# Kernel optimization log

Hardware: AMD Instinct MI355X
Metric: run time of the kernel (lower is better)

## Reference

```python
import jax, jax.numpy as jnp
import numpy as np


def setup_inputs() -> dict:
    key = jax.random.key(0)
    k1, k2 = jax.random.split(key)
    B, H, W = 16, 1024, 1024
    NB = 20
    preds = jax.random.randint(k1, (B, H, W), 0, NB, dtype=jnp.int32)
    targets = jax.random.randint(k2, (B, H, W), 0, NB, dtype=jnp.int32)
    return {"preds": preds, "targets": targets, "nb_class": NB, "smooth": 1}


def reference(preds, targets, nb_class, smooth):
    # Single-pass histogram formulation of the per-class IoU loop:
    #   intersection[c] = #{pred==c and target==c}
    #   union[c]        = #{pred==c} + #{target==c} - intersection[c]
    p = preds.reshape(-1)
    t = targets.reshape(-1)
    pred_count = jnp.bincount(p, length=nb_class).astype(jnp.float32)
    target_count = jnp.bincount(t, length=nb_class).astype(jnp.float32)
    # pixels where pred==target contribute to intersection of that class
    match = p == t
    intersection = jnp.bincount(jnp.where(match, p, nb_class), length=nb_class + 1)[:nb_class].astype(jnp.float32)
    union = pred_count + target_count - intersection
    s = jnp.float32(smooth)
    iou_per_class = (intersection + s) / (union + s)  # [nb_class]
    mIoU = iou_per_class.mean()
    return 1.0 - mIoU
```

## Files before the change

kernel.cpp:

```cpp
#include <hip/hip_runtime.h>
#include <hip/hip_bf16.h>


#define NB      20
#define BLK     256
#define GRID_H  1024
#define PSTRIDE 64

__device__ __forceinline__ void dma16(const void* g, void* l) {
    __builtin_amdgcn_global_load_lds(
        (const __attribute__((address_space(1))) unsigned*)g,
        (__attribute__((address_space(3))) unsigned*)l, 16, 0, 0);
}

__device__ __forceinline__ void process_pix(int p, int t, unsigned* s_col) {
    unsigned m = (unsigned)(p == t);
    atomicAdd(&s_col[p * BLK], 1u + (m << 20));
    atomicAdd(&s_col[t * BLK], 1u << 10);
}

__device__ __forceinline__ void process_vec(int4 pv, int4 tv, unsigned* s_col) {
    process_pix(pv.x, tv.x, s_col);
    process_pix(pv.y, tv.y, s_col);
    process_pix(pv.z, tv.z, s_col);
    process_pix(pv.w, tv.w, s_col);
}

__global__ __launch_bounds__(BLK) void miou_hist_kernel(
        const int4* __restrict__ preds, const int4* __restrict__ targs,
        unsigned* __restrict__ partials, int n4, int full_iters) {
    __shared__ unsigned s_hist[NB * BLK];
    __shared__ int4 s_p[2][BLK];
    __shared__ int4 s_t[2][BLK];
    const int tid  = threadIdx.x;
    const int wid  = tid >> 6;
    const int lane = tid & 63;

    #pragma unroll
    for (int c = 0; c < NB; ++c) s_hist[c * BLK + tid] = 0u;
    __syncthreads();

    unsigned* s_col = &s_hist[tid];
    const int CHUNK = gridDim.x * BLK;
    const int base  = blockIdx.x * BLK + tid;

    if (full_iters >= 2) {
        dma16(&preds[base],         &s_p[0][wid * 64]);
        dma16(&targs[base],         &s_t[0][wid * 64]);
        dma16(&preds[base + CHUNK], &s_p[1][wid * 64]);
        dma16(&targs[base + CHUNK], &s_t[1][wid * 64]);

        for (int j = 0; j < full_iters - 1; ++j) {
            const int slot = j & 1;
            asm volatile("s_waitcnt vmcnt(2)" ::: "memory");
            int4 pv = s_p[slot][wid * 64 + lane];
            int4 tv = s_t[slot][wid * 64 + lane];
            asm volatile("s_waitcnt lgkmcnt(0)" ::: "memory");
            if (j + 2 < full_iters) {
                dma16(&preds[base + (j + 2) * CHUNK], &s_p[slot][wid * 64]);
                dma16(&targs[base + (j + 2) * CHUNK], &s_t[slot][wid * 64]);
            }
            process_vec(pv, tv, s_col);
        }
        {
            const int slot = (full_iters - 1) & 1;
            asm volatile("s_waitcnt vmcnt(0)" ::: "memory");
            int4 pv = s_p[slot][wid * 64 + lane];
            int4 tv = s_t[slot][wid * 64 + lane];
            process_vec(pv, tv, s_col);
        }
    }
    for (int i = base + full_iters * CHUNK; i < n4; i += CHUNK) {
        int4 pv = preds[i];
        int4 tv = targs[i];
        process_vec(pv, tv, s_col);
    }
    __syncthreads();

    unsigned* dst = &partials[(size_t)blockIdx.x * PSTRIDE];
    for (int c = wid; c < NB; c += (BLK / 64)) {
        unsigned sp = 0, st = 0, si = 0;
        #pragma unroll
        for (int k = 0; k < BLK / 64; ++k) {
            unsigned v = s_hist[c * BLK + k * 64 + lane];
            sp += v & 1023u;
            st += (v >> 10) & 1023u;
            si += (v >> 20) & 1023u;
        }
        #pragma unroll
        for (int off = 32; off > 0; off >>= 1) {
            sp += __shfl_xor(sp, off);
            st += __shfl_xor(st, off);
            si += __shfl_xor(si, off);
        }
        if (lane == 0) {
            dst[c]          = sp;
            dst[NB + c]     = st;
            dst[2 * NB + c] = si;
        }
    }
}

__global__ __launch_bounds__(1024) void miou_reduce_kernel(
        const unsigned* __restrict__ partials, int nblocks,
        const int* __restrict__ nb_ptr, const int* __restrict__ smooth_ptr,
        float* __restrict__ out) {
    __shared__ unsigned s_tot[PSTRIDE];
    if (threadIdx.x < PSTRIDE) s_tot[threadIdx.x] = 0u;
    __syncthreads();

    const int col4 = threadIdx.x & 15;
    const int seg  = threadIdx.x >> 4;
    const int4* p4 = (const int4*)partials;

    unsigned ax = 0, ay = 0, az = 0, aw = 0;
    #pragma unroll 8
    for (int r = seg; r < nblocks; r += 64) {
        int4 v = p4[r * 16 + col4];
        ax += (unsigned)v.x; ay += (unsigned)v.y;
        az += (unsigned)v.z; aw += (unsigned)v.w;
    }
    atomicAdd(&s_tot[col4 * 4 + 0], ax);
    atomicAdd(&s_tot[col4 * 4 + 1], ay);
    atomicAdd(&s_tot[col4 * 4 + 2], az);
    atomicAdd(&s_tot[col4 * 4 + 3], aw);
    __syncthreads();

    if (threadIdx.x == 0) {
        const int   nb = *nb_ptr;
        const float s  = (float)(*smooth_ptr);
        float acc_iou = 0.0f;
        for (int c = 0; c < nb && c < NB; ++c) {
            float pc    = (float)s_tot[c];
            float tc    = (float)s_tot[NB + c];
            float inter = (float)s_tot[2 * NB + c];
            float uni   = pc + tc - inter;
            acc_iou += (inter + s) / (uni + s);
        }
        out[0] = 1.0f - acc_iou / (float)nb;
    }
}

extern "C" void kernel_launch(void* const* d_in, const int* in_sizes, int n_in,
                              void* d_out, int out_size, void* d_ws, size_t ws_size,
                              hipStream_t stream) {
    const int4* preds      = (const int4*)d_in[0];
    const int4* targs      = (const int4*)d_in[1];
    const int*  nb_ptr     = (const int*)d_in[2];
    const int*  smooth_ptr = (const int*)d_in[3];
    float*      out        = (float*)d_out;

    int n  = in_sizes[0];
    int n4 = n >> 2;

    unsigned* partials = (unsigned*)d_ws;

    int grid = GRID_H;
    int max_grid = (n4 + BLK - 1) / BLK;
    if (grid > max_grid) grid = max_grid;
    size_t need_per_block = PSTRIDE * sizeof(unsigned);
    if ((size_t)grid * need_per_block > ws_size)
        grid = (int)(ws_size / need_per_block);

    int chunk = grid * BLK;
    int full  = n4 / chunk;
    if (full < 2) full = 0;

    miou_hist_kernel<<<grid, BLK, 0, stream>>>(preds, targs, partials, n4, full);
    miou_reduce_kernel<<<1, 1024, 0, stream>>>(partials, grid, nb_ptr, smooth_ptr, out);
}
```

Baseline: 34.63 us.

## Switch to joint pred-target histogram with replicated LDS copies

Replaces the two packed per-thread-column atomics per pixel with a single LDS atomic into a 20x20 joint (pred,target) histogram, replicated 32 ways by lane. Pred, target and intersection counts are then recovered from row sums, column sums and the diagonal during the final block reduction. This halves the LDS atomic count per pixel, but 32 copies means lanes from the two halves of a wave share a copy, so some atomic contention is possible. The grid is also halved to 512 blocks, giving each block more iterations and making the reduction cost a smaller share of the work.

```diff
diff --git a/kernel.cpp b/kernel.cpp
--- a/kernel.cpp
+++ b/kernel.cpp
@@ -3,8 +3,10 @@
 
 
 #define NB      20
+#define NKEY    (NB * NB)
+#define NCOPY   32
 #define BLK     256
-#define GRID_H  1024
+#define GRID_H  512
 #define PSTRIDE 64
 
 __device__ __forceinline__ void dma16(const void* g, void* l) {
@@ -13,34 +15,31 @@
         (__attribute__((address_space(3))) unsigned*)l, 16, 0, 0);
 }
 
-__device__ __forceinline__ void process_pix(int p, int t, unsigned* s_col) {
-    unsigned m = (unsigned)(p == t);
-    atomicAdd(&s_col[p * BLK], 1u + (m << 20));
-    atomicAdd(&s_col[t * BLK], 1u << 10);
+__device__ __forceinline__ void process_pix(int p, int t, unsigned* hist_cp) {
+    atomicAdd(&hist_cp[(p * NB + t) * NCOPY], 1u);
 }
 
-__device__ __forceinline__ void process_vec(int4 pv, int4 tv, unsigned* s_col) {
-    process_pix(pv.x, tv.x, s_col);
-    process_pix(pv.y, tv.y, s_col);
-    process_pix(pv.z, tv.z, s_col);
-    process_pix(pv.w, tv.w, s_col);
+__device__ __forceinline__ void process_vec(int4 pv, int4 tv, unsigned* hist_cp) {
+    process_pix(pv.x, tv.x, hist_cp);
+    process_pix(pv.y, tv.y, hist_cp);
+    process_pix(pv.z, tv.z, hist_cp);
+    process_pix(pv.w, tv.w, hist_cp);
 }
 
 __global__ __launch_bounds__(BLK) void miou_hist_kernel(
         const int4* __restrict__ preds, const int4* __restrict__ targs,
         unsigned* __restrict__ partials, int n4, int full_iters) {
-    __shared__ unsigned s_hist[NB * BLK];
+    __shared__ unsigned s_hist[NKEY * NCOPY];
     __shared__ int4 s_p[2][BLK];
     __shared__ int4 s_t[2][BLK];
     const int tid  = threadIdx.x;
     const int wid  = tid >> 6;
     const int lane = tid & 63;
 
-    #pragma unroll
-    for (int c = 0; c < NB; ++c) s_hist[c * BLK + tid] = 0u;
+    for (int k = tid; k < NKEY * NCOPY; k += BLK) s_hist[k] = 0u;
     __syncthreads();
 
-    unsigned* s_col = &s_hist[tid];
+    unsigned* hist_cp = &s_hist[tid & (NCOPY - 1)];
     const int CHUNK = gridDim.x * BLK;
     const int base  = blockIdx.x * BLK + tid;
 
@@ -60,43 +59,49 @@
                 dma16(&preds[base + (j + 2) * CHUNK], &s_p[slot][wid * 64]);
                 dma16(&targs[base + (j + 2) * CHUNK], &s_t[slot][wid * 64]);
             }
-            process_vec(pv, tv, s_col);
+            process_vec(pv, tv, hist_cp);
         }
         {
             const int slot = (full_iters - 1) & 1;
             asm volatile("s_waitcnt vmcnt(0)" ::: "memory");
             int4 pv = s_p[slot][wid * 64 + lane];
             int4 tv = s_t[slot][wid * 64 + lane];
-            process_vec(pv, tv, s_col);
+            process_vec(pv, tv, hist_cp);
         }
     }
     for (int i = base + full_iters * CHUNK; i < n4; i += CHUNK) {
         int4 pv = preds[i];
         int4 tv = targs[i];
-        process_vec(pv, tv, s_col);
+        process_vec(pv, tv, hist_cp);
     }
     __syncthreads();
 
     unsigned* dst = &partials[(size_t)blockIdx.x * PSTRIDE];
     for (int c = wid; c < NB; c += (BLK / 64)) {
-        unsigned sp = 0, st = 0, si = 0;
+        unsigned pcs = 0;
         #pragma unroll
-        for (int k = 0; k < BLK / 64; ++k) {
-            unsigned v = s_hist[c * BLK + k * 64 + lane];
-            sp += v & 1023u;
-            st += (v >> 10) & 1023u;
-            si += (v >> 20) & 1023u;
+        for (int k = 0; k < 640; k += 64) pcs += s_hist[c * 640 + k + lane];
+
+        unsigned tcs = 0;
+        {
+            const int copy = lane & 31;
+            const int p0   = lane >> 5;
+            #pragma unroll
+            for (int p = 0; p < NB; p += 2)
+                tcs += s_hist[(p + p0) * 640 + c * 32 + copy];
         }
+        unsigned ics = (lane < 32) ? s_hist[c * 21 * 32 + lane] : 0u;
+
         #pragma unroll
         for (int off = 32; off > 0; off >>= 1) {
-            sp += __shfl_xor(sp, off);
-            st += __shfl_xor(st, off);
-            si += __shfl_xor(si, off);
+            pcs += __shfl_xor(pcs, off);
+            tcs += __shfl_xor(tcs, off);
+            ics += __shfl_xor(ics, off);
         }
         if (lane == 0) {
-            dst[c]          = sp;
-            dst[NB + c]     = st;
-            dst[2 * NB + c] = si;
+            dst[c]          = pcs;
+            dst[NB + c]     = tcs;
+            dst[2 * NB + c] = ics;
         }
     }
 }
@@ -163,7 +168,7 @@
         grid = (int)(ws_size / need_per_block);
 
     int chunk = grid * BLK;
-    int full  = n4 / chunk;
+    int full  = (chunk > 0) ? (n4 / chunk) : 0;
     if (full < 2) full = 0;
 
     miou_hist_kernel<<<grid, BLK, 0, stream>>>(preds, targs, partials, n4, full);
```

Result: faster. 32.69 us (-5.6%).
